# Performance work log

Hardware: AMD Instinct MI355X
Metric: run time of the kernel (lower is better)

Reference implementation:

```python
import jax, jax.numpy as jnp
import numpy as np

N_NODES = 100000
N_EDGES = 3200000
IN_F, HID, OUT = 24, 64, 1


def _gcn_conv(x, W, b, src, dst, norm, n):
    # x: [N, Fin] -> h: [N, Fout]; PyG GCNConv: lin first, then normalized aggregation, then bias
    h = x @ W                                    # [N, Fout]
    msg = h[src] * norm[:, None]                 # [E+N, Fout] gathered, norm-weighted messages
    agg = jax.ops.segment_sum(msg, dst, num_segments=n)  # scatter-add to targets
    return agg + b


def setup_inputs() -> dict:
    key = jax.random.key(0)
    k1, k2, k3, k4 = jax.random.split(key, 4)
    x = jax.random.normal(k1, (N_NODES, IN_F), dtype=jnp.float32)
    edge_index = jax.random.randint(k2, (2, N_EDGES), 0, N_NODES, dtype=jnp.int64)
    # Glorot-ish init for weights
    W1 = jax.random.normal(k3, (IN_F, HID), dtype=jnp.float32) / np.sqrt(IN_F)
    b1 = jnp.zeros((HID,), dtype=jnp.float32)
    W2 = jax.random.normal(k4, (HID, OUT), dtype=jnp.float32) / np.sqrt(HID)
    b2 = jnp.zeros((OUT,), dtype=jnp.float32)
    return {"x": x, "edge_index": edge_index, "W1": W1, "b1": b1, "W2": W2, "b2": b2}


def reference(x, edge_index, W1, b1, W2, b2):
    n = x.shape[0]
    # add self-loops (PyG GCNConv default)
    loops = jnp.arange(n, dtype=edge_index.dtype)
    src = jnp.concatenate([edge_index[0], loops])
    dst = jnp.concatenate([edge_index[1], loops])
    # symmetric normalization: deg over targets of A+I, norm_e = d^-1/2[src] * d^-1/2[dst]
    deg = jax.ops.segment_sum(jnp.ones_like(dst, dtype=x.dtype), dst, num_segments=n)
    dinv = jnp.where(deg > 0, jax.lax.rsqrt(deg), 0.0)
    norm = dinv[src] * dinv[dst]
    h = _gcn_conv(x, W1, b1, src, dst, norm, n)
    h = jax.nn.relu(h)
    # F.dropout with training=self.training -> identity in eval mode (reference runs eval)
    out = _gcn_conv(h, W2, b2, src, dst, norm, n)
    return out
```

## Files before the change

### kernel.cpp

```cpp
#include <hip/hip_runtime.h>
#include <hip/hip_fp16.h>

#define IN_F 24
#define HID 64
#define NB 512
#define NPB 512
#define GSZ_MAX 256
#define PBUF 7168
#define SRC_BITS 17

typedef unsigned int u32;


__device__ __forceinline__ int bucket_lo(int b, int n) {
    return (int)(((long long)b * n + NB - 1) / NB);
}

__global__ __launch_bounds__(1024) void k_pcount(const int* __restrict__ dst,
                                                 u32* __restrict__ pc, int e, int n) {
    __shared__ u32 h[NB];
    for (int j = threadIdx.x; j < NB; j += 1024) h[j] = 0;
    __syncthreads();
    int blk = blockIdx.x;
    long long begin = (long long)e * blk / NPB;
    long long end   = (long long)e * (blk + 1) / NPB;
    for (long long i = begin + threadIdx.x; i < end; i += 1024) {
        int k = (int)((long long)dst[i] * NB / n);
        atomicAdd(&h[k], 1u);
    }
    __syncthreads();
    for (int j = threadIdx.x; j < NB; j += 1024) pc[(size_t)blk * NB + j] = h[j];
}

__global__ __launch_bounds__(256) void k_pscan_a(u32* __restrict__ pc,
                                                 u32* __restrict__ colsum) {
    __shared__ u32 ps[256];
    int t = blockIdx.x;
    int tid = threadIdx.x;
    u32 v0 = pc[(size_t)(2 * tid) * NB + t];
    u32 v1 = pc[(size_t)(2 * tid + 1) * NB + t];
    u32 tsum = v0 + v1;
    ps[tid] = tsum;
    __syncthreads();
    for (int off = 1; off < 256; off <<= 1) {
        u32 v2 = (tid >= off) ? ps[tid - off] : 0;
        __syncthreads();
        ps[tid] += v2;
        __syncthreads();
    }
    u32 excl = ps[tid] - tsum;
    pc[(size_t)(2 * tid) * NB + t] = excl;
    pc[(size_t)(2 * tid + 1) * NB + t] = excl + v0;
    if (tid == 255) colsum[t] = ps[255];
}

__global__ void k_pscan_b(const u32* __restrict__ colsum, u32* __restrict__ basep) {
    __shared__ u32 s[NB];
    int t = threadIdx.x;
    u32 v = colsum[t];
    s[t] = v;
    __syncthreads();
    for (int off = 1; off < NB; off <<= 1) {
        u32 v2 = (t >= off) ? s[t - off] : 0;
        __syncthreads();
        s[t] += v2;
        __syncthreads();
    }
    basep[t] = s[t] - v;
}

__global__ __launch_bounds__(1024) void k_part(const int* __restrict__ src,
                                               const int* __restrict__ dst,
                                               const u32* __restrict__ pc,
                                               const u32* __restrict__ basep,
                                               u32* __restrict__ pairs, int e, int n) {
    __shared__ u32 cur[NB];
    int blk = (blockIdx.x & 7) * (NPB / 8) + (blockIdx.x >> 3);
    for (int j = threadIdx.x; j < NB; j += 1024)
        cur[j] = pc[(size_t)blk * NB + j] + basep[j];
    __syncthreads();
    long long begin = (long long)e * blk / NPB;
    long long end   = (long long)e * (blk + 1) / NPB;
    for (long long i = begin + threadIdx.x; i < end; i += 1024) {
        int d = dst[i];
        int sv = src[i];
        int k = (int)((long long)d * NB / n);
        u32 loc = (u32)(d - bucket_lo(k, n));
        u32 pos = atomicAdd(&cur[k], 1u);
        pairs[pos] = (loc << SRC_BITS) | (u32)sv;
    }
}

__global__ __launch_bounds__(1024) void k_bucket(const u32* __restrict__ pairs,
                                                 const u32* __restrict__ basep,
                                                 const float* __restrict__ x,
                                                 int* __restrict__ cnt,
                                                 int* __restrict__ row_start,
                                                 float* __restrict__ dinv,
                                                 int* __restrict__ csr_src,
                                                 __half2* __restrict__ xs2, int e, int n) {
    __shared__ u32 pbuf[PBUF];
    __shared__ u32 h[GSZ_MAX];
    __shared__ u32 cur[GSZ_MAX];
    __shared__ u32 sc[GSZ_MAX];
    __shared__ float dloc[GSZ_MAX];
    int b = blockIdx.x;
    if (b == 0 && threadIdx.x < 12)
        xs2[(long long)n * 12 + threadIdx.x] = __floats2half2_rn(0.0f, 0.0f);
    int lo = bucket_lo(b, n);
    int hi = bucket_lo(b + 1, n);
    int gsz = hi - lo;
    u32 start = basep[b];
    u32 endp = (b + 1 < NB) ? basep[b + 1] : (u32)e;
    int nbp = (int)(endp - start);
    for (int j = threadIdx.x; j < GSZ_MAX; j += 1024) h[j] = 0;
    __syncthreads();
    int stored = nbp < PBUF ? nbp : PBUF;
    for (int i = threadIdx.x; i < stored; i += 1024) {
        u32 p = pairs[start + i];
        pbuf[i] = p;
        atomicAdd(&h[p >> SRC_BITS], 1u);
    }
    for (int i = PBUF + threadIdx.x; i < nbp; i += 1024) {
        atomicAdd(&h[pairs[start + i] >> SRC_BITS], 1u);
    }
    __syncthreads();
    int t = threadIdx.x;
    u32 v = 0;
    if (t < GSZ_MAX) { v = h[t]; sc[t] = v; }
    __syncthreads();
    for (int off = 1; off < GSZ_MAX; off <<= 1) {
        u32 v2 = (t >= off && t < GSZ_MAX) ? sc[t - off] : 0;
        __syncthreads();
        if (t < GSZ_MAX) sc[t] += v2;
        __syncthreads();
    }
    u32 excl = (t < GSZ_MAX) ? (sc[t] - v) : 0;
    if (t < gsz) {
        float dv = rsqrtf((float)(v + 1));
        cnt[lo + t] = (int)v;
        row_start[lo + t] = (int)(start + excl);
        dinv[lo + t] = dv;
        dloc[t] = dv;
        cur[t] = excl;
    }
    __syncthreads();
    for (int i = threadIdx.x; i < stored; i += 1024) {
        u32 p = pbuf[i];
        u32 pos = atomicAdd(&cur[p >> SRC_BITS], 1u);
        csr_src[start + pos] = (int)(p & ((1u << SRC_BITS) - 1));
    }
    for (int i = PBUF + threadIdx.x; i < nbp; i += 1024) {
        u32 p = pairs[start + i];
        u32 pos = atomicAdd(&cur[p >> SRC_BITS], 1u);
        csr_src[start + pos] = (int)(p & ((1u << SRC_BITS) - 1));
    }
    const float2* xf = (const float2*)(x + (long long)lo * IN_F);
    for (int i = threadIdx.x; i < gsz * 12; i += 1024) {
        float2 vv = xf[i];
        float dn = dloc[i / 12];
        xs2[(long long)lo * 12 + i] = __floats2half2_rn(vv.x * dn, vv.y * dn);
    }
}

__global__ __launch_bounds__(256) void k_agg_hz(const float* __restrict__ x,
                                                const __half2* __restrict__ xs2,
                                                const float* __restrict__ dinv,
                                                const int* __restrict__ row_start,
                                                const int* __restrict__ cnt,
                                                const int* __restrict__ csr_src,
                                                const float* __restrict__ W1,
                                                const float* __restrict__ b1,
                                                const float* __restrict__ W2,
                                                float* __restrict__ zs, int n) {
    __shared__ float w[IN_F * HID];
    __shared__ float w2s[HID];
    __shared__ float b1s[HID];
    for (int j = threadIdx.x; j < IN_F * HID; j += 256) w[j] = W1[j];
    if (threadIdx.x < HID) { w2s[threadIdx.x] = W2[threadIdx.x]; b1s[threadIdx.x] = b1[threadIdx.x]; }
    __syncthreads();
    int g = threadIdx.x >> 3;
    int f4 = threadIdx.x & 7;
    int node = blockIdx.x * 32 + g;
    if (node >= n) return;
    float dn = dinv[node];
    const uint2* xq = (const uint2*)xs2;
    float ax0 = 0.0f, ay0 = 0.0f, ax1 = 0.0f, ay1 = 0.0f;
    if (f4 < 6) {
        int row = row_start[node];
        int c = cnt[node];
        float a0 = 0.0f, b0 = 0.0f, c0 = 0.0f, d0 = 0.0f;
        float a1 = 0.0f, b1v = 0.0f, c1 = 0.0f, d1 = 0.0f;
        int j = 0;
        for (; j + 16 <= c; j += 16) {
            const int* cp = csr_src + row + j;
            int s[16];
#pragma unroll
            for (int t = 0; t < 16; ++t) s[t] = cp[t];
            uint2 u[16];
#pragma unroll
            for (int t = 0; t < 16; ++t) u[t] = xq[(size_t)((u32)s[t] * 6u + (u32)f4)];
#pragma unroll
            for (int t = 0; t < 16; t += 2) {
                float2 e0 = __half22float2(__builtin_bit_cast(__half2, u[t].x));
                float2 e1 = __half22float2(__builtin_bit_cast(__half2, u[t].y));
                float2 o0 = __half22float2(__builtin_bit_cast(__half2, u[t + 1].x));
                float2 o1 = __half22float2(__builtin_bit_cast(__half2, u[t + 1].y));
                a0 += e0.x; b0 += e0.y; c0 += e1.x; d0 += e1.y;
                a1 += o0.x; b1v += o0.y; c1 += o1.x; d1 += o1.y;
            }
        }
        if (j < c) {
            const int* cp = csr_src + row + j;
            int rem = c - j;
            int s[16];
#pragma unroll
            for (int t = 0; t < 16; ++t) {
                int tmp = cp[t];
                s[t] = (t < rem) ? tmp : n;
            }
            uint2 u[16];
#pragma unroll
            for (int t = 0; t < 16; ++t) u[t] = xq[(size_t)((u32)s[t] * 6u + (u32)f4)];
#pragma unroll
            for (int t = 0; t < 16; t += 2) {
                float2 e0 = __half22float2(__builtin_bit_cast(__half2, u[t].x));
                float2 e1 = __half22float2(__builtin_bit_cast(__half2, u[t].y));
                float2 o0 = __half22float2(__builtin_bit_cast(__half2, u[t + 1].x));
                float2 o1 = __half22float2(__builtin_bit_cast(__half2, u[t + 1].y));
                a0 += e0.x; b0 += e0.y; c0 += e1.x; d0 += e1.y;
                a1 += o0.x; b1v += o0.y; c1 += o1.x; d1 += o1.y;
            }
        }
        ax0 = a0 + a1; ay0 = b0 + b1v; ax1 = c0 + c1; ay1 = d0 + d1;
        float4 sx4 = *(const float4*)(x + (long long)node * IN_F + 4 * f4);
        ax0 = (ax0 + sx4.x * dn) * dn;
        ay0 = (ay0 + sx4.y * dn) * dn;
        ax1 = (ax1 + sx4.z * dn) * dn;
        ay1 = (ay1 + sx4.w * dn) * dn;
    }
    int fb = f4 * 8;
    float h[8];
#pragma unroll
    for (int jj = 0; jj < 8; ++jj) h[jj] = b1s[fb + jj];
#pragma unroll
    for (int k = 0; k < IN_F; ++k) {
        int sl = k >> 2;
        int r = k & 3;
        float xv;
        if (r == 0)      xv = __shfl(ax0, sl, 8);
        else if (r == 1) xv = __shfl(ay0, sl, 8);
        else if (r == 2) xv = __shfl(ax1, sl, 8);
        else             xv = __shfl(ay1, sl, 8);
        const float* wr = w + k * HID + fb;
#pragma unroll
        for (int jj = 0; jj < 8; ++jj) h[jj] += xv * wr[jj];
    }
    float p = 0.0f;
#pragma unroll
    for (int jj = 0; jj < 8; ++jj) p += fmaxf(h[jj], 0.0f) * w2s[fb + jj];
    p += __shfl_down(p, 4, 8);
    p += __shfl_down(p, 2, 8);
    p += __shfl_down(p, 1, 8);
    if (f4 == 0) zs[node] = p * dn;
}

__global__ void k_out(const float* __restrict__ zs, const float* __restrict__ dinv,
                      const int* __restrict__ row_start, const int* __restrict__ cnt,
                      const int* __restrict__ csr_src, const float* __restrict__ b2,
                      float* __restrict__ out, int n) {
    int t = blockIdx.x * blockDim.x + threadIdx.x;
    int node = t >> 4;
    int lane = t & 15;
    if (node >= n) return;
    int row = row_start[node];
    int c = cnt[node];
    float v = 0.0f;
    for (int j = lane; j < c; j += 16) {
        v += zs[csr_src[row + j]];
    }
    v += __shfl_down(v, 8, 16);
    v += __shfl_down(v, 4, 16);
    v += __shfl_down(v, 2, 16);
    v += __shfl_down(v, 1, 16);
    if (lane == 0) {
        out[node] = b2[0] + dinv[node] * (zs[node] + v);
    }
}

extern "C" void kernel_launch(void* const* d_in, const int* in_sizes, int n_in,
                              void* d_out, int out_size, void* d_ws, size_t ws_size,
                              hipStream_t stream) {
    const float* x   = (const float*)d_in[0];
    const int*   ei  = (const int*)d_in[1];
    const float* W1  = (const float*)d_in[2];
    const float* b1  = (const float*)d_in[3];
    const float* W2  = (const float*)d_in[4];
    const float* b2  = (const float*)d_in[5];
    float* out = (float*)d_out;

    const int n = in_sizes[0] / IN_F;
    const int e = in_sizes[1] / 2;
    const int* src = ei;
    const int* dst = ei + e;

    const int B = 256;

    char* base = (char*)d_ws;
    u32* pairs     = (u32*)base;
    float* zs      = (float*)base;
    size_t ov = ((size_t)e * 4 + 255) & ~(size_t)255;
    char* after    = base + ov;
    int* cnt       = (int*)after;
    int* row_start = cnt + n;
    int* csr_src   = row_start + n;
    float* dinv    = (float*)(csr_src + e);
    __half* xs     = (__half*)(dinv + n);
    u32* pc        = (u32*)(xs + (size_t)(n + 1) * IN_F);
    u32* colsum    = pc + (size_t)NPB * NB;
    u32* basep     = colsum + NB;

    k_pcount<<<NPB, 1024, 0, stream>>>(dst, pc, e, n);
    k_pscan_a<<<NB, B, 0, stream>>>(pc, colsum);
    k_pscan_b<<<1, NB, 0, stream>>>(colsum, basep);
    k_part<<<NPB, 1024, 0, stream>>>(src, dst, pc, basep, pairs, e, n);
    k_bucket<<<NB, 1024, 0, stream>>>(pairs, basep, x, cnt, row_start, dinv, csr_src,
                                      (__half2*)xs, e, n);

    k_agg_hz<<<(n + 31) / 32, B, 0, stream>>>(x, (const __half2*)xs, dinv,
                                              row_start, cnt, csr_src,
                                              W1, b1, W2, zs, n);

    const long long n16 = (long long)n * 16;
    k_out<<<(int)((n16 + B - 1) / B), B, 0, stream>>>(zs, dinv, row_start, cnt, csr_src, b2, out, n);
}
```

Baseline: 189.5 us.

## Replace count-and-scan partitioning with fixed-capacity sub-buckets via global atomic cursors

The separate count kernel and the two prefix-scan kernels are removed. Edges are now scattered directly into fixed-capacity slots per (bucket, group) using global atomic cursors, so the sort no longer needs an extra pass over dst or the scan launches. The bucket kernel derives each bucket's offsets from the eight group cursors. The CSR then uses a padded layout with a fixed stride per bucket. This adds global atomic contention and silently relies on no sub-bucket ever exceeding its fixed capacity, which holds only for roughly uniform degree distributions.

```diff
diff --git a/kernel.cpp b/kernel.cpp
--- a/kernel.cpp
+++ b/kernel.cpp
@@ -5,6 +5,9 @@
 #define HID 64
 #define NB 512
 #define NPB 512
+#define NG 8
+#define SUBCAP 1568
+#define BCAP (NG * SUBCAP)
 #define GSZ_MAX 256
 #define PBUF 7168
 #define SRC_BITS 17
@@ -16,69 +19,12 @@
     return (int)(((long long)b * n + NB - 1) / NB);
 }
 
-__global__ __launch_bounds__(1024) void k_pcount(const int* __restrict__ dst,
-                                                 u32* __restrict__ pc, int e, int n) {
-    __shared__ u32 h[NB];
-    for (int j = threadIdx.x; j < NB; j += 1024) h[j] = 0;
-    __syncthreads();
-    int blk = blockIdx.x;
-    long long begin = (long long)e * blk / NPB;
-    long long end   = (long long)e * (blk + 1) / NPB;
-    for (long long i = begin + threadIdx.x; i < end; i += 1024) {
-        int k = (int)((long long)dst[i] * NB / n);
-        atomicAdd(&h[k], 1u);
-    }
-    __syncthreads();
-    for (int j = threadIdx.x; j < NB; j += 1024) pc[(size_t)blk * NB + j] = h[j];
-}
-
-__global__ __launch_bounds__(256) void k_pscan_a(u32* __restrict__ pc,
-                                                 u32* __restrict__ colsum) {
-    __shared__ u32 ps[256];
-    int t = blockIdx.x;
-    int tid = threadIdx.x;
-    u32 v0 = pc[(size_t)(2 * tid) * NB + t];
-    u32 v1 = pc[(size_t)(2 * tid + 1) * NB + t];
-    u32 tsum = v0 + v1;
-    ps[tid] = tsum;
-    __syncthreads();
-    for (int off = 1; off < 256; off <<= 1) {
-        u32 v2 = (tid >= off) ? ps[tid - off] : 0;
-        __syncthreads();
-        ps[tid] += v2;
-        __syncthreads();
-    }
-    u32 excl = ps[tid] - tsum;
-    pc[(size_t)(2 * tid) * NB + t] = excl;
-    pc[(size_t)(2 * tid + 1) * NB + t] = excl + v0;
-    if (tid == 255) colsum[t] = ps[255];
-}
-
-__global__ void k_pscan_b(const u32* __restrict__ colsum, u32* __restrict__ basep) {
-    __shared__ u32 s[NB];
-    int t = threadIdx.x;
-    u32 v = colsum[t];
-    s[t] = v;
-    __syncthreads();
-    for (int off = 1; off < NB; off <<= 1) {
-        u32 v2 = (t >= off) ? s[t - off] : 0;
-        __syncthreads();
-        s[t] += v2;
-        __syncthreads();
-    }
-    basep[t] = s[t] - v;
-}
-
 __global__ __launch_bounds__(1024) void k_part(const int* __restrict__ src,
                                                const int* __restrict__ dst,
-                                               const u32* __restrict__ pc,
-                                               const u32* __restrict__ basep,
+                                               u32* __restrict__ cursor,
                                                u32* __restrict__ pairs, int e, int n) {
-    __shared__ u32 cur[NB];
-    int blk = (blockIdx.x & 7) * (NPB / 8) + (blockIdx.x >> 3);
-    for (int j = threadIdx.x; j < NB; j += 1024)
-        cur[j] = pc[(size_t)blk * NB + j] + basep[j];
-    __syncthreads();
+    int blk = blockIdx.x;
+    int g = blk & (NG - 1);
     long long begin = (long long)e * blk / NPB;
     long long end   = (long long)e * (blk + 1) / NPB;
     for (long long i = begin + threadIdx.x; i < end; i += 1024) {
@@ -86,13 +32,13 @@
         int sv = src[i];
         int k = (int)((long long)d * NB / n);
         u32 loc = (u32)(d - bucket_lo(k, n));
-        u32 pos = atomicAdd(&cur[k], 1u);
-        pairs[pos] = (loc << SRC_BITS) | (u32)sv;
+        u32 pos = atomicAdd(&cursor[g * NB + k], 1u);
+        pairs[(size_t)(k * NG + g) * SUBCAP + pos] = (loc << SRC_BITS) | (u32)sv;
     }
 }
 
 __global__ __launch_bounds__(1024) void k_bucket(const u32* __restrict__ pairs,
-                                                 const u32* __restrict__ basep,
+                                                 const u32* __restrict__ cursor,
                                                  const float* __restrict__ x,
                                                  int* __restrict__ cnt,
                                                  int* __restrict__ row_start,
@@ -104,28 +50,33 @@
     __shared__ u32 cur[GSZ_MAX];
     __shared__ u32 sc[GSZ_MAX];
     __shared__ float dloc[GSZ_MAX];
+    __shared__ u32 goff[NG + 1];
     int b = blockIdx.x;
-    if (b == 0 && threadIdx.x < 12)
-        xs2[(long long)n * 12 + threadIdx.x] = __floats2half2_rn(0.0f, 0.0f);
+    int t = threadIdx.x;
+    if (b == 0 && t < 12)
+        xs2[(long long)n * 12 + t] = __floats2half2_rn(0.0f, 0.0f);
     int lo = bucket_lo(b, n);
     int hi = bucket_lo(b + 1, n);
     int gsz = hi - lo;
-    u32 start = basep[b];
-    u32 endp = (b + 1 < NB) ? basep[b + 1] : (u32)e;
-    int nbp = (int)(endp - start);
-    for (int j = threadIdx.x; j < GSZ_MAX; j += 1024) h[j] = 0;
-    __syncthreads();
-    int stored = nbp < PBUF ? nbp : PBUF;
-    for (int i = threadIdx.x; i < stored; i += 1024) {
-        u32 p = pairs[start + i];
-        pbuf[i] = p;
-        atomicAdd(&h[p >> SRC_BITS], 1u);
-    }
-    for (int i = PBUF + threadIdx.x; i < nbp; i += 1024) {
-        atomicAdd(&h[pairs[start + i] >> SRC_BITS], 1u);
-    }
-    __syncthreads();
-    int t = threadIdx.x;
+    for (int j = t; j < GSZ_MAX; j += 1024) h[j] = 0;
+    if (t == 0) {
+        u32 acc = 0;
+        for (int g = 0; g < NG; ++g) { goff[g] = acc; acc += cursor[g * NB + b]; }
+        goff[NG] = acc;
+    }
+    __syncthreads();
+    for (int g = 0; g < NG; ++g) {
+        u32 off = goff[g];
+        int cg = (int)(goff[g + 1] - off);
+        const u32* pg = pairs + (size_t)(b * NG + g) * SUBCAP;
+        for (int i = t; i < cg; i += 1024) {
+            u32 p = pg[i];
+            int idx = (int)off + i;
+            if (idx < PBUF) pbuf[idx] = p;
+            atomicAdd(&h[p >> SRC_BITS], 1u);
+        }
+    }
+    __syncthreads();
     u32 v = 0;
     if (t < GSZ_MAX) { v = h[t]; sc[t] = v; }
     __syncthreads();
@@ -136,6 +87,7 @@
         __syncthreads();
     }
     u32 excl = (t < GSZ_MAX) ? (sc[t] - v) : 0;
+    u32 start = (u32)b * BCAP;
     if (t < gsz) {
         float dv = rsqrtf((float)(v + 1));
         cnt[lo + t] = (int)v;
@@ -145,18 +97,19 @@
         cur[t] = excl;
     }
     __syncthreads();
-    for (int i = threadIdx.x; i < stored; i += 1024) {
-        u32 p = pbuf[i];
-        u32 pos = atomicAdd(&cur[p >> SRC_BITS], 1u);
-        csr_src[start + pos] = (int)(p & ((1u << SRC_BITS) - 1));
-    }
-    for (int i = PBUF + threadIdx.x; i < nbp; i += 1024) {
-        u32 p = pairs[start + i];
-        u32 pos = atomicAdd(&cur[p >> SRC_BITS], 1u);
-        csr_src[start + pos] = (int)(p & ((1u << SRC_BITS) - 1));
+    for (int g = 0; g < NG; ++g) {
+        u32 off = goff[g];
+        int cg = (int)(goff[g + 1] - off);
+        const u32* pg = pairs + (size_t)(b * NG + g) * SUBCAP;
+        for (int i = t; i < cg; i += 1024) {
+            int idx = (int)off + i;
+            u32 p = (idx < PBUF) ? pbuf[idx] : pg[i];
+            u32 pos = atomicAdd(&cur[p >> SRC_BITS], 1u);
+            csr_src[start + pos] = (int)(p & ((1u << SRC_BITS) - 1));
+        }
     }
     const float2* xf = (const float2*)(x + (long long)lo * IN_F);
-    for (int i = threadIdx.x; i < gsz * 12; i += 1024) {
+    for (int i = t; i < gsz * 12; i += 1024) {
         float2 vv = xf[i];
         float dn = dloc[i / 12];
         xs2[(long long)lo * 12 + i] = __floats2half2_rn(vv.x * dn, vv.y * dn);
@@ -309,22 +262,18 @@
     char* base = (char*)d_ws;
     u32* pairs     = (u32*)base;
     float* zs      = (float*)base;
-    size_t ov = ((size_t)e * 4 + 255) & ~(size_t)255;
+    size_t ov = ((size_t)NB * BCAP * 4 + 255) & ~(size_t)255;
     char* after    = base + ov;
     int* cnt       = (int*)after;
     int* row_start = cnt + n;
     int* csr_src   = row_start + n;
-    float* dinv    = (float*)(csr_src + e);
+    float* dinv    = (float*)(csr_src + (size_t)NB * BCAP);
     __half* xs     = (__half*)(dinv + n);
-    u32* pc        = (u32*)(xs + (size_t)(n + 1) * IN_F);
-    u32* colsum    = pc + (size_t)NPB * NB;
-    u32* basep     = colsum + NB;
-
-    k_pcount<<<NPB, 1024, 0, stream>>>(dst, pc, e, n);
-    k_pscan_a<<<NB, B, 0, stream>>>(pc, colsum);
-    k_pscan_b<<<1, NB, 0, stream>>>(colsum, basep);
-    k_part<<<NPB, 1024, 0, stream>>>(src, dst, pc, basep, pairs, e, n);
-    k_bucket<<<NB, 1024, 0, stream>>>(pairs, basep, x, cnt, row_start, dinv, csr_src,
+    u32* cursor    = (u32*)(xs + (size_t)(n + 1) * IN_F);
+
+    hipMemsetAsync(cursor, 0, (size_t)NG * NB * sizeof(u32), stream);
+    k_part<<<NPB, 1024, 0, stream>>>(src, dst, cursor, pairs, e, n);
+    k_bucket<<<NB, 1024, 0, stream>>>(pairs, cursor, x, cnt, row_start, dinv, csr_src,
                                       (__half2*)xs, e, n);
 
     k_agg_hz<<<(n + 31) / 32, B, 0, stream>>>(x, (const __half2*)xs, dinv,
```

After: 395.2 us. +108.6%, slower.
